# Kernel tuning notes

Measured on AMD Instinct MI355X. Metric: run time of the kernel, lower is better.

## Reference

```python
import jax, jax.numpy as jnp
import numpy as np

T, B, OBS, H, P, L, A = 512, 128, 512, 256, 128, 4, 4


def _ln(x, scale, bias, eps=1e-6):
    mu = jnp.mean(x, axis=-1, keepdims=True)
    var = jnp.mean((x - mu) ** 2, axis=-1, keepdims=True)
    return (x - mu) * jax.lax.rsqrt(var + eps) * scale + bias


def _binop(qi, qj):
    # S5 reset-aware associative operator: elements (A, b, reset_flag)
    Ai, bi, ci = qi
    Aj, bj, cj = qj
    A = (Aj * Ai) * (1.0 - cj) + Aj * cj
    b = (Aj * bi + bj) * (1.0 - cj) + bj * cj
    c = ci * (1.0 - cj) + cj
    return A, b, c


def _s5_layer(x, dones, h0, scale, bias, lam_re, lam_im, b_re, b_im, c_re, c_im, d_vec, log_step, glu_W, glu_b):
    # x: (T,B,H) real, dones: (T,B), h0: (B,P) complex64
    skip = x
    u = _ln(x, scale, bias)                                  # prenorm
    lam = lam_re + 1j * lam_im                               # (P,)
    step = jnp.exp(log_step)                                 # (P,)
    lam_bar = jnp.exp(lam * step)                            # ZOH discretization
    B_bar = ((lam_bar - 1.0) / lam)[:, None] * (b_re + 1j * b_im)  # (P,H)
    Bu = jnp.einsum('tbh,ph->tbp', u.astype(jnp.complex64), B_bar)  # (T,B,P)
    A_el = jnp.concatenate([jnp.ones((1, B, P), jnp.complex64),
                            jnp.broadcast_to(lam_bar.astype(jnp.complex64), (T, B, P))], axis=0)
    b_el = jnp.concatenate([h0[None], Bu], axis=0)
    c_el = jnp.concatenate([jnp.zeros((1, B, 1), jnp.float32), dones[..., None]], axis=0)
    _, xs, _ = jax.lax.associative_scan(_binop, (A_el, b_el, c_el), axis=0)
    xs = xs[1:]                                              # (T,B,P) complex states
    new_h = xs[-1]
    C = c_re + 1j * c_im                                     # (H,P)
    ys = 2.0 * jnp.real(jnp.einsum('tbp,hp->tbh', xs, C)) + d_vec * u  # conj_sym output + D*u
    z = _ln(ys, scale, bias)                                 # gtrxl norm (shared LayerNorm params)
    z = jax.nn.gelu(z)                                       # half_glu1
    z = z * jax.nn.sigmoid(z @ glu_W + glu_b)
    return skip + z, new_h


def setup_inputs() -> dict:
    key = jax.random.key(0)
    ks = jax.random.split(key, 40)
    f32 = jnp.float32

    def n(i, shape, s=1.0):
        return jax.random.normal(ks[i], shape, f32) * s

    inp = {}
    inp['obs'] = n(0, (T, B, OBS))
    inp['dones'] = (jax.random.uniform(ks[1], (T, B)) < 0.01).astype(f32)
    inp['hidden_re'] = jnp.zeros((L, B, P), f32)
    inp['hidden_im'] = jnp.zeros((L, B, P), f32)
    inp['enc0_W'] = n(2, (OBS, 128), 1.0 / np.sqrt(OBS))
    inp['enc0_b'] = jnp.zeros((128,), f32)
    inp['enc1_W'] = n(3, (128, H), 1.0 / np.sqrt(128))
    inp['enc1_b'] = jnp.zeros((H,), f32)
    inp['norm_scale'] = jnp.ones((L, H), f32)
    inp['norm_bias'] = jnp.zeros((L, H), f32)
    inp['Lambda_re'] = -0.5 * jax.random.uniform(ks[4], (L, P), f32) - 0.1
    inp['Lambda_im'] = n(5, (L, P), np.pi)
    inp['B_re'] = n(6, (L, P, H), 1.0 / np.sqrt(H))
    inp['B_im'] = n(7, (L, P, H), 1.0 / np.sqrt(H))
    inp['C_re'] = n(8, (L, H, P), 1.0 / np.sqrt(2 * P))
    inp['C_im'] = n(9, (L, H, P), 1.0 / np.sqrt(2 * P))
    inp['D'] = n(10, (L, H))
    inp['log_step'] = jax.random.uniform(ks[11], (L, P), f32, np.log(1e-3), np.log(1e-1))
    inp['glu_W'] = n(12, (L, H, H), 1.0 / np.sqrt(H))
    inp['glu_b'] = jnp.zeros((L, H), f32)
    inp['ab0_W'] = n(13, (H, 128), 1.0 / np.sqrt(H))
    inp['ab0_b'] = jnp.zeros((128,), f32)
    inp['ab1_W'] = n(14, (128, 128), 1.0 / np.sqrt(128))
    inp['ab1_b'] = jnp.zeros((128,), f32)
    inp['adec_W'] = n(15, (128, A), 0.01 / np.sqrt(128))
    inp['adec_b'] = jnp.full((A,), 0.5, f32)
    inp['log_std'] = jnp.full((A,), -0.7, f32)
    inp['vb0_W'] = n(16, (H, 128), 1.0 / np.sqrt(H))
    inp['vb0_b'] = jnp.zeros((128,), f32)
    inp['vb1_W'] = n(17, (128, 128), 1.0 / np.sqrt(128))
    inp['vb1_b'] = jnp.zeros((128,), f32)
    inp['vdec_W'] = n(18, (128, 1), 1.0 / np.sqrt(128))
    inp['vdec_b'] = jnp.zeros((1,), f32)
    return inp


def reference(obs, dones, hidden_re, hidden_im, enc0_W, enc0_b, enc1_W, enc1_b,
              norm_scale, norm_bias, Lambda_re, Lambda_im, B_re, B_im, C_re, C_im,
              D, log_step, glu_W, glu_b, ab0_W, ab0_b, ab1_W, ab1_b, adec_W, adec_b,
              log_std, vb0_W, vb0_b, vb1_W, vb1_b, vdec_W, vdec_b):
    e = jax.nn.leaky_relu(obs @ enc0_W + enc0_b)
    e = jax.nn.leaky_relu(e @ enc1_W + enc1_b)
    h0 = (hidden_re + 1j * hidden_im).astype(jnp.complex64)  # (L,B,P)
    new_h = []
    for l in range(L):
        e, hl = _s5_layer(e, dones, h0[l], norm_scale[l], norm_bias[l],
                          Lambda_re[l], Lambda_im[l], B_re[l], B_im[l],
                          C_re[l], C_im[l], D[l], log_step[l], glu_W[l], glu_b[l])
        new_h.append(hl)
    new_h = jnp.stack(new_h)
    am = jax.nn.leaky_relu(e @ ab0_W + ab0_b)
    am = jax.nn.leaky_relu(am @ ab1_W + ab1_b)
    am = am @ adec_W + adec_b                                # actor mean (T,B,A)
    v = jax.nn.leaky_relu(e @ vb0_W + vb0_b)
    v = jax.nn.leaky_relu(v @ vb1_W + vb1_b)
    v = v @ vdec_W + vdec_b                                  # critic (T,B,1)
    sc = jnp.broadcast_to(jnp.exp(log_std), am.shape)        # Normal scale (pi params)
    out = jnp.concatenate([am, sc, v], axis=-1)              # (T,B,2A+1)
    return out, jnp.real(new_h), jnp.imag(new_h)
```

## Files before the change

kernel.cpp:

```cpp
#include <hip/hip_runtime.h>
#include <math.h>

#define TT 512
#define BB 128
#define OBSD 512
#define HD 256
#define PD 128
#define LD 4
#define NTB (TT*BB)

typedef __bf16 bf16x8 __attribute__((ext_vector_type(8)));
typedef float  f32x4  __attribute__((ext_vector_type(4)));

__device__ __forceinline__ float bf2f(unsigned short u) {
    return __uint_as_float(((unsigned)u) << 16);
}
__device__ __forceinline__ unsigned short f2bf(float f) {
    unsigned u = __float_as_uint(f);
    unsigned r = (u + 0x7FFFu + ((u >> 16) & 1u)) >> 16;
    return (unsigned short)r;
}
__device__ __forceinline__ float gelu_f(float x) {
    float x3 = x * x * x;
    return 0.5f * x * (1.f + tanhf(0.7978845608028654f * (x + 0.044715f * x3)));
}

template<int MODE, int NJ>
__global__ __launch_bounds__(256, 4) void mgemm2(
    const unsigned short* __restrict__ A, const unsigned short* __restrict__ BT,
    int K, int LDA, const float* __restrict__ bias,
    const float* __restrict__ lnsc, const float* __restrict__ lnbi,
    const unsigned short* __restrict__ aux1, unsigned short* Xio,
    unsigned short* __restrict__ U, int wU)
{
    const int N = NJ * 64;
    __shared__ unsigned short smA[2][64 * 32];
    __shared__ unsigned short smB[2][NJ * 64 * 32];
    float2 (*red)[4] = reinterpret_cast<float2(*)[4]>(&smA[0][0]);
    int tid = threadIdx.x;
    int lane = tid & 63, w = tid >> 6;
    int m16 = lane & 15, quad = lane >> 4;
    int m0 = blockIdx.x * 64;

    f32x4 acc[4][NJ] = {};

    auto stage = [&](int bu, int k0) {
        const unsigned short* g = A + (size_t)(m0 + (tid >> 2)) * LDA + k0 + (tid & 3) * 8;
        __builtin_amdgcn_global_load_lds(
            (const __attribute__((address_space(1))) void*)g,
            (__attribute__((address_space(3))) void*)(&smA[bu][0] + tid * 8), 16, 0, 0);
#pragma unroll
        for (int p = 0; p < NJ; ++p) {
            const unsigned short* gb = BT + (size_t)(p * 64 + (tid >> 2)) * K + k0 + (tid & 3) * 8;
            __builtin_amdgcn_global_load_lds(
                (const __attribute__((address_space(1))) void*)gb,
                (__attribute__((address_space(3))) void*)(&smB[bu][0] + p * 2048 + tid * 8), 16, 0, 0);
        }
    };

    int nk = K >> 5;
    stage(0, 0);
    for (int t = 0; t < nk; ++t) {
        int cur = t & 1;
        if (t + 1 < nk) {
            stage(cur ^ 1, (t + 1) << 5);
            asm volatile("s_waitcnt vmcnt(%0)" :: "i"(NJ + 1) : "memory");
        } else {
            asm volatile("s_waitcnt vmcnt(0)" ::: "memory");
        }
        __builtin_amdgcn_s_barrier();
        __builtin_amdgcn_sched_barrier(0);
        bf16x8 af[4], bfr[NJ];
#pragma unroll
        for (int mi = 0; mi < 4; ++mi)
            af[mi] = *(const bf16x8*)(&smA[cur][0] + (mi * 16 + m16) * 32 + quad * 8);
#pragma unroll
        for (int nj = 0; nj < NJ; ++nj)
            bfr[nj] = *(const bf16x8*)(&smB[cur][0] + (w * NJ * 16 + nj * 16 + m16) * 32 + quad * 8);
#pragma unroll
        for (int mi = 0; mi < 4; ++mi)
#pragma unroll
            for (int nj = 0; nj < NJ; ++nj)
                acc[mi][nj] = __builtin_amdgcn_mfma_f32_16x16x32_bf16(
                    bfr[nj], af[mi], acc[mi][nj], 0, 0, 0);
        __builtin_amdgcn_sched_barrier(0);
        __builtin_amdgcn_s_barrier();
    }

    int colb = w * NJ * 16 + quad * 4;

    if (MODE == 1) {
#pragma unroll
        for (int mi = 0; mi < 4; ++mi) {
            size_t rowb = (size_t)(m0 + mi * 16 + m16) * N;
#pragma unroll
            for (int nj = 0; nj < NJ; ++nj) {
                ushort4 o = { f2bf(acc[mi][nj][0]), f2bf(acc[mi][nj][1]),
                              f2bf(acc[mi][nj][2]), f2bf(acc[mi][nj][3]) };
                *(ushort4*)(U + rowb + colb + nj * 16) = o;
            }
        }
        return;
    }

#pragma unroll
    for (int mi = 0; mi < 4; ++mi) {
        size_t rowb = (size_t)(m0 + mi * 16 + m16) * N;
        float s = 0.f, q = 0.f;
#pragma unroll
        for (int nj = 0; nj < NJ; ++nj) {
            float4 bn = *(const float4*)(bias + colb + nj * 16);
            ushort4 a1, xo;
            if (MODE == 2 || MODE == 3) a1 = *(const ushort4*)(aux1 + rowb + colb + nj * 16);
            if (MODE == 3)              xo = *(const ushort4*)(Xio + rowb + colb + nj * 16);
            float vv[4];
#pragma unroll
            for (int r = 0; r < 4; ++r) {
                float v = acc[mi][nj][r];
                float bv = (r == 0) ? bn.x : (r == 1) ? bn.y : (r == 2) ? bn.z : bn.w;
                if (MODE == 0 || MODE == 4) {
                    v += bv; v = v > 0.f ? v : 0.01f * v;
                } else if (MODE == 2) {
                    float u = bf2f(r == 0 ? a1.x : r == 1 ? a1.y : r == 2 ? a1.z : a1.w);
                    v += bv * u;
                } else if (MODE == 3) {
                    float zz = bf2f(r == 0 ? a1.x : r == 1 ? a1.y : r == 2 ? a1.z : a1.w);
                    float xx = bf2f(r == 0 ? xo.x : r == 1 ? xo.y : r == 2 ? xo.z : xo.w);
                    float sg = 1.f / (1.f + expf(-(v + bv)));
                    v = xx + zz * sg;
                }
                vv[r] = v;
                acc[mi][nj][r] = v;
                s += v; q += v * v;
            }
            if (MODE == 0 || MODE == 3) {
                ushort4 o = { f2bf(vv[0]), f2bf(vv[1]), f2bf(vv[2]), f2bf(vv[3]) };
                *(ushort4*)(Xio + rowb + colb + nj * 16) = o;
            } else if (MODE == 4) {
                ushort4 o = { f2bf(vv[0]), f2bf(vv[1]), f2bf(vv[2]), f2bf(vv[3]) };
                *(ushort4*)(U + rowb + colb + nj * 16) = o;
            }
        }
        if (MODE != 4 && (MODE != 3 || wU)) {
            s += __shfl_xor(s, 16); q += __shfl_xor(q, 16);
            s += __shfl_xor(s, 32); q += __shfl_xor(q, 32);
            if (quad == 0) red[mi * 16 + m16][w] = float2{s, q};
        }
    }
    if (MODE == 4 || (MODE == 3 && !wU)) return;
    __syncthreads();

#pragma unroll
    for (int mi = 0; mi < 4; ++mi) {
        int row_l = mi * 16 + m16;
        float2 t0 = red[row_l][0], t1 = red[row_l][1], t2 = red[row_l][2], t3 = red[row_l][3];
        float S = t0.x + t1.x + t2.x + t3.x;
        float Q = t0.y + t1.y + t2.y + t3.y;
        float mu = S * (1.f / 256.f);
        float var = Q * (1.f / 256.f) - mu * mu;
        float rstd = rsqrtf(var + 1e-6f);
        size_t rowb = (size_t)(m0 + row_l) * N;
#pragma unroll
        for (int nj = 0; nj < NJ; ++nj) {
            float4 ls = *(const float4*)(lnsc + colb + nj * 16);
            float4 lb = *(const float4*)(lnbi + colb + nj * 16);
            float o[4];
#pragma unroll
            for (int r = 0; r < 4; ++r) {
                float sc = (r == 0) ? ls.x : (r == 1) ? ls.y : (r == 2) ? ls.z : ls.w;
                float bi = (r == 0) ? lb.x : (r == 1) ? lb.y : (r == 2) ? lb.z : lb.w;
                float v = (acc[mi][nj][r] - mu) * rstd * sc + bi;
                if (MODE == 2) v = gelu_f(v);
                o[r] = v;
            }
            ushort4 ov = { f2bf(o[0]), f2bf(o[1]), f2bf(o[2]), f2bf(o[3]) };
            *(ushort4*)(U + rowb + colb + nj * 16) = ov;
        }
    }
}

__global__ __launch_bounds__(256, 4) void mgemm_obs(
    const float* __restrict__ A, const unsigned short* __restrict__ BT,
    unsigned short* __restrict__ U, const float* __restrict__ bias)
{
    const int K = 512, NJ = 2, N = 128;
    __shared__ unsigned short smA[64 * 32];
    __shared__ unsigned short smB[NJ * 64 * 32];
    int tid = threadIdx.x;
    int lane = tid & 63, w = tid >> 6;
    int m16 = lane & 15, quad = lane >> 4;
    int m0 = blockIdx.x * 64;

    f32x4 acc[4][NJ] = {};
    for (int k0 = 0; k0 < K; k0 += 32) {
#pragma unroll
        for (int p = 0; p < 2; ++p) {
            int idx = p * 256 + tid;
            int r = idx >> 3, kq = (idx & 7) * 4;
            float4 v = *(const float4*)(A + (size_t)(m0 + r) * K + k0 + kq);
            ushort4 o = { f2bf(v.x), f2bf(v.y), f2bf(v.z), f2bf(v.w) };
            *(ushort4*)(smA + r * 32 + kq) = o;
        }
#pragma unroll
        for (int p = 0; p < NJ; ++p) {
            const unsigned short* g = BT + (size_t)(p * 64 + (tid >> 2)) * K + k0 + (tid & 3) * 8;
            unsigned short* l = smB + p * 2048 + tid * 8;
            __builtin_amdgcn_global_load_lds(
                (const __attribute__((address_space(1))) void*)g,
                (__attribute__((address_space(3))) void*)l, 16, 0, 0);
        }
        __syncthreads();
        bf16x8 af[4], bfr[NJ];
#pragma unroll
        for (int mi = 0; mi < 4; ++mi)
            af[mi] = *(const bf16x8*)(smA + (mi * 16 + m16) * 32 + quad * 8);
#pragma unroll
        for (int nj = 0; nj < NJ; ++nj)
            bfr[nj] = *(const bf16x8*)(smB + (w * NJ * 16 + nj * 16 + m16) * 32 + quad * 8);
#pragma unroll
        for (int mi = 0; mi < 4; ++mi)
#pragma unroll
            for (int nj = 0; nj < NJ; ++nj)
                acc[mi][nj] = __builtin_amdgcn_mfma_f32_16x16x32_bf16(
                    bfr[nj], af[mi], acc[mi][nj], 0, 0, 0);
        __syncthreads();
    }
    int colb = w * NJ * 16 + quad * 4;
#pragma unroll
    for (int mi = 0; mi < 4; ++mi) {
        size_t rowb = (size_t)(m0 + mi * 16 + m16) * N;
#pragma unroll
        for (int nj = 0; nj < NJ; ++nj) {
            float4 bv = *(const float4*)(bias + colb + nj * 16);
            float v0 = acc[mi][nj][0] + bv.x; v0 = v0 > 0.f ? v0 : 0.01f * v0;
            float v1 = acc[mi][nj][1] + bv.y; v1 = v1 > 0.f ? v1 : 0.01f * v1;
            float v2 = acc[mi][nj][2] + bv.z; v2 = v2 > 0.f ? v2 : 0.01f * v2;
            float v3 = acc[mi][nj][3] + bv.w; v3 = v3 > 0.f ? v3 : 0.01f * v3;
            ushort4 o = { f2bf(v0), f2bf(v1), f2bf(v2), f2bf(v3) };
            *(ushort4*)(U + rowb + colb + nj * 16) = o;
        }
    }
}

__global__ __launch_bounds__(512) void scan2_k(
    const unsigned short* __restrict__ bu, unsigned short* __restrict__ xs,
    const float* __restrict__ dones,
    const float* __restrict__ h0re, const float* __restrict__ h0im,
    const float* __restrict__ lamre, const float* __restrict__ lamim,
    const float* __restrict__ lstep,
    float* __restrict__ outre, float* __restrict__ outim)
{
    __shared__ float sdone[TT];
    __shared__ float4 ssum[8][64];
    __shared__ float2 shin[8][64];
    int tid = threadIdx.x;
    int b  = blockIdx.x >> 1;
    int ph = blockIdx.x & 1;
    int chunk = tid >> 6, pl = tid & 63;
    int p = ph * 64 + pl;
    sdone[tid] = dones[tid * BB + b];
    float lr = lamre[p], li = lamim[p];
    float st = expf(lstep[p]);
    float er = expf(lr * st);
    float ar = er * cosf(li * st);
    float ai = er * sinf(li * st);
    __syncthreads();

    int t0 = chunk * 64;
    unsigned buf[64];
    float Ar = 1.f, Ai = 0.f, br = 0.f, bi = 0.f;
#pragma unroll
    for (int j = 0; j < 64; ++j) {
        size_t off = ((size_t)(t0 + j) * BB + b) * 256 + 2 * p;
        unsigned v = *(const unsigned*)(bu + off);
        buf[j] = v;
        float bur = bf2f((unsigned short)(v & 0xFFFFu));
        float bui = bf2f((unsigned short)(v >> 16));
        if (sdone[t0 + j] != 0.f) {
            Ar = 0.f; Ai = 0.f; br = bur; bi = bui;
        } else {
            float nAr = ar * Ar - ai * Ai;
            float nAi = ar * Ai + ai * Ar;
            float nbr = fmaf(ar, br, fmaf(-ai, bi, bur));
            float nbi = fmaf(ar, bi, fmaf(ai, br, bui));
            Ar = nAr; Ai = nAi; br = nbr; bi = nbi;
        }
    }
    ssum[chunk][pl] = float4{Ar, Ai, br, bi};
    __syncthreads();
    if (tid < 64) {
        int gid = b * 128 + p;
        float hr = h0re[gid], hi = h0im[gid];
#pragma unroll
        for (int c = 0; c < 8; ++c) {
            shin[c][pl] = float2{hr, hi};
            float4 s = ssum[c][pl];
            float nhr = fmaf(s.x, hr, fmaf(-s.y, hi, s.z));
            float nhi = fmaf(s.x, hi, fmaf(s.y, hr, s.w));
            hr = nhr; hi = nhi;
        }
        outre[gid] = hr; outim[gid] = hi;
    }
    __syncthreads();
    float hr = shin[chunk][pl].x, hi = shin[chunk][pl].y;
#pragma unroll
    for (int j = 0; j < 64; ++j) {
        unsigned v = buf[j];
        float bur = bf2f((unsigned short)(v & 0xFFFFu));
        float bui = bf2f((unsigned short)(v >> 16));
        float nr, ni;
        if (sdone[t0 + j] != 0.f) { nr = bur; ni = bui; }
        else {
            nr = fmaf(ar, hr, fmaf(-ai, hi, bur));
            ni = fmaf(ar, hi, fmaf(ai, hr, bui));
        }
        hr = nr; hi = ni;
        size_t off = ((size_t)(t0 + j) * BB + b) * 256 + 2 * p;
        *(unsigned*)(xs + off) = ((unsigned)f2bf(ni) << 16) | f2bf(nr);
    }
}

__global__ __launch_bounds__(256) void prep_k(
    const float* __restrict__ Br, const float* __restrict__ Bi,
    const float* __restrict__ Cr, const float* __restrict__ Ci,
    const float* __restrict__ Lr, const float* __restrict__ Li,
    const float* __restrict__ ls, unsigned short* bbarT, unsigned short* ccatT)
{
    int gid = blockIdx.x * 256 + threadIdx.x;
    int l = gid >> 15;
    int rem = gid & 32767;
    int p = rem >> 8;
    int h = rem & 255;
    float lr = Lr[l * PD + p], li = Li[l * PD + p];
    float st = expf(ls[l * PD + p]);
    float er = expf(lr * st);
    float lbr = er * cosf(li * st);
    float lbi = er * sinf(li * st);
    float nr = lbr - 1.f, ni = lbi;
    float den = lr * lr + li * li;
    float fr = (nr * lr + ni * li) / den;
    float fi = (ni * lr - nr * li) / den;
    float bre = Br[(size_t)(l * PD + p) * HD + h];
    float bim = Bi[(size_t)(l * PD + p) * HD + h];
    size_t lb = (size_t)l * 65536;
    bbarT[lb + (size_t)(2 * p) * 256 + h]     = f2bf(fr * bre - fi * bim);
    bbarT[lb + (size_t)(2 * p + 1) * 256 + h] = f2bf(fr * bim + fi * bre);
    float cre = Cr[(size_t)(l * HD + h) * PD + p];
    float cim = Ci[(size_t)(l * HD + h) * PD + p];
    ccatT[lb + (size_t)h * 256 + 2 * p]     = f2bf(2.f * cre);
    ccatT[lb + (size_t)h * 256 + 2 * p + 1] = f2bf(-2.f * cim);
}

__global__ __launch_bounds__(256) void tcvt_k(const float* __restrict__ in,
    unsigned short* __restrict__ out, int K, int N)
{
    int gid = blockIdx.x * 256 + threadIdx.x;
    if (gid >= K * N) return;
    int k = gid / N, n = gid - k * N;
    out[(size_t)n * K + k] = f2bf(in[gid]);
}

__global__ __launch_bounds__(256) void tcvt4_k(const float* __restrict__ in,
    unsigned short* __restrict__ out)
{
    int gid = blockIdx.x * 256 + threadIdx.x;
    int l = gid >> 16;
    int rem = gid & 65535;
    int k = rem >> 8, n = rem & 255;
    out[(size_t)l * 65536 + (size_t)n * 256 + k] = f2bf(in[gid]);
}

__global__ __launch_bounds__(256) void catb_k(const float* __restrict__ a,
    const float* __restrict__ b, float* __restrict__ out)
{
    int i = threadIdx.x;
    out[i] = (i < 128) ? a[i] : b[i - 128];
}

__global__ __launch_bounds__(256) void head_k(
    const unsigned short* __restrict__ am2, const unsigned short* __restrict__ v2,
    const float* __restrict__ adW, const float* __restrict__ adb,
    const float* __restrict__ lstd,
    const float* __restrict__ vdW, const float* __restrict__ vdb,
    float* out)
{
    int wid = threadIdx.x >> 6, lane = threadIdx.x & 63;
    size_t row = (size_t)blockIdx.x * 4 + wid;
    float a1 = bf2f(am2[row * 128 + lane]);
    float a2 = bf2f(am2[row * 128 + 64 + lane]);
    float w1 = bf2f(v2[row * 128 + lane]);
    float w2 = bf2f(v2[row * 128 + 64 + lane]);
    float vals[5];
#pragma unroll
    for (int a = 0; a < 4; ++a)
        vals[a] = a1 * adW[lane * 4 + a] + a2 * adW[(lane + 64) * 4 + a];
    vals[4] = w1 * vdW[lane] + w2 * vdW[64 + lane];
#pragma unroll
    for (int off = 32; off; off >>= 1)
#pragma unroll
        for (int k = 0; k < 5; ++k) vals[k] += __shfl_xor(vals[k], off);
    if (lane == 0) {
        size_t o = row * 9;
#pragma unroll
        for (int a = 0; a < 4; ++a) out[o + a] = vals[a] + adb[a];
#pragma unroll
        for (int a = 0; a < 4; ++a) out[o + 4 + a] = expf(lstd[a]);
        out[o + 8] = vals[4] + vdb[0];
    }
}

extern "C" void kernel_launch(void* const* d_in, const int* in_sizes, int n_in,
                              void* d_out, int out_size, void* d_ws, size_t ws_size,
                              hipStream_t stream) {
    (void)in_sizes; (void)n_in; (void)out_size; (void)ws_size;
    const float* obs     = (const float*)d_in[0];
    const float* dones   = (const float*)d_in[1];
    const float* hre     = (const float*)d_in[2];
    const float* him     = (const float*)d_in[3];
    const float* enc0_W  = (const float*)d_in[4];
    const float* enc0_b  = (const float*)d_in[5];
    const float* enc1_W  = (const float*)d_in[6];
    const float* enc1_b  = (const float*)d_in[7];
    const float* nsc     = (const float*)d_in[8];
    const float* nbi     = (const float*)d_in[9];
    const float* Lre     = (const float*)d_in[10];
    const float* Lim     = (const float*)d_in[11];
    const float* B_re    = (const float*)d_in[12];
    const float* B_im    = (const float*)d_in[13];
    const float* C_re    = (const float*)d_in[14];
    const float* C_im    = (const float*)d_in[15];
    const float* Dv      = (const float*)d_in[16];
    const float* lstep   = (const float*)d_in[17];
    const float* glu_W   = (const float*)d_in[18];
    const float* glu_b   = (const float*)d_in[19];
    const float* ab0_W   = (const float*)d_in[20];
    const float* ab0_b   = (const float*)d_in[21];
    const float* ab1_W   = (const float*)d_in[22];
    const float* ab1_b   = (const float*)d_in[23];
    const float* adec_W  = (const float*)d_in[24];
    const float* adec_b  = (const float*)d_in[25];
    const float* log_std = (const float*)d_in[26];
    const float* vb0_W   = (const float*)d_in[27];
    const float* vb0_b   = (const float*)d_in[28];
    const float* vb1_W   = (const float*)d_in[29];
    const float* vb1_b   = (const float*)d_in[30];
    const float* vdec_W  = (const float*)d_in[31];
    const float* vdec_b  = (const float*)d_in[32];

    const size_t MB = (size_t)1 << 20;
    char* wsb = (char*)d_ws;
    unsigned short* XS    = (unsigned short*)(wsb);
    unsigned short* AMV1  = (unsigned short*)(wsb);
    unsigned short* AM2   = (unsigned short*)(wsb + 32 * MB);
    unsigned short* V2    = (unsigned short*)(wsb + 48 * MB);
    unsigned short* U1    = (unsigned short*)(wsb + 64 * MB);
    unsigned short* X     = (unsigned short*)(wsb + 96 * MB);
    unsigned short* U     = (unsigned short*)(wsb + 128 * MB);
    unsigned short* BU    = (unsigned short*)(wsb + 160 * MB);
    char* wgt = wsb + 192 * MB;
    unsigned short* BBART = (unsigned short*)(wgt);
    unsigned short* CCATT = (unsigned short*)(wgt + 512 * 1024);
    unsigned short* GLUT  = (unsigned short*)(wgt + 1024 * 1024);
    unsigned short* E0T   = (unsigned short*)(wgt + 1536 * 1024);
    unsigned short* E1T   = (unsigned short*)(wgt + 1664 * 1024);
    unsigned short* AB0VT = (unsigned short*)(wgt + 1728 * 1024);
    unsigned short* AB1T  = (unsigned short*)(wgt + 1856 * 1024);
    unsigned short* VB1T  = (unsigned short*)(wgt + 1888 * 1024);
    float*          CB0   = (float*)(wgt + 1920 * 1024);

    float* out   = (float*)d_out;
    float* outre = out + (size_t)NTB * 9;
    float* outim = outre + LD * BB * PD;

    prep_k<<<512, 256, 0, stream>>>(B_re, B_im, C_re, C_im, Lre, Lim, lstep, BBART, CCATT);
    tcvt_k<<<256, 256, 0, stream>>>(enc0_W, E0T, 512, 128);
    tcvt_k<<<128, 256, 0, stream>>>(enc1_W, E1T, 128, 256);
    tcvt4_k<<<1024, 256, 0, stream>>>(glu_W, GLUT);
    tcvt_k<<<128, 256, 0, stream>>>(ab0_W, AB0VT, 256, 128);
    tcvt_k<<<128, 256, 0, stream>>>(vb0_W, AB0VT + 128 * 256, 256, 128);
    tcvt_k<<<64, 256, 0, stream>>>(ab1_W, AB1T, 128, 128);
    tcvt_k<<<64, 256, 0, stream>>>(vb1_W, VB1T, 128, 128);
    catb_k<<<1, 256, 0, stream>>>(ab0_b, vb0_b, CB0);

    mgemm_obs<<<1024, 256, 0, stream>>>(obs, E0T, U1, enc0_b);
    mgemm2<0, 4><<<1024, 256, 0, stream>>>(U1, E1T, 128, 128, enc1_b, nsc, nbi, nullptr, X, U, 1);

    for (int l = 0; l < LD; ++l) {
        mgemm2<1, 4><<<1024, 256, 0, stream>>>(U, BBART + (size_t)l * 65536, 256, 256,
                                               nullptr, nullptr, nullptr, nullptr, nullptr, BU, 0);
        scan2_k<<<256, 512, 0, stream>>>(BU, XS, dones, hre + l * BB * PD, him + l * BB * PD,
                                         Lre + l * PD, Lim + l * PD, lstep + l * PD,
                                         outre + l * BB * PD, outim + l * BB * PD);
        mgemm2<2, 4><<<1024, 256, 0, stream>>>(XS, CCATT + (size_t)l * 65536, 256, 256,
                                               Dv + l * HD, nsc + l * HD, nbi + l * HD, U, nullptr, U, 1);
        const float* nsc2 = nsc + ((l + 1 < LD) ? (l + 1) * HD : 0);
        const float* nbi2 = nbi + ((l + 1 < LD) ? (l + 1) * HD : 0);
        mgemm2<3, 4><<<1024, 256, 0, stream>>>(U, GLUT + (size_t)l * 65536, 256, 256,
                                               glu_b + l * HD, nsc2, nbi2, U, X, U, (l + 1 < LD) ? 1 : 0);
    }

    mgemm2<4, 4><<<1024, 256, 0, stream>>>(X, AB0VT, 256, 256, CB0, nullptr, nullptr, nullptr, nullptr, AMV1, 0);
    mgemm2<4, 2><<<1024, 256, 0, stream>>>(AMV1, AB1T, 128, 256, ab1_b, nullptr, nullptr, nullptr, nullptr, AM2, 0);
    mgemm2<4, 2><<<1024, 256, 0, stream>>>(AMV1 + 128, VB1T, 128, 256, vb1_b, nullptr, nullptr, nullptr, nullptr, V2, 0);
    head_k<<<NTB / 4, 256, 0, stream>>>(AM2, V2, adec_W, adec_b, log_std, vdec_W, vdec_b, out);
}
```

Before: 1.048 ms.

## Use 8-wave GEMM blocks with triple-buffered LDS prefetch

Result: faster. 960.5 us (-8.4%).

```diff
diff --git a/kernel.cpp b/kernel.cpp
--- a/kernel.cpp
+++ b/kernel.cpp
@@ -26,75 +26,95 @@
 }
 
 template<int MODE, int NJ>
-__global__ __launch_bounds__(256, 4) void mgemm2(
+__global__ __launch_bounds__(512) void mgemm2(
     const unsigned short* __restrict__ A, const unsigned short* __restrict__ BT,
     int K, int LDA, const float* __restrict__ bias,
     const float* __restrict__ lnsc, const float* __restrict__ lnbi,
     const unsigned short* __restrict__ aux1, unsigned short* Xio,
     unsigned short* __restrict__ U, int wU)
 {
+    constexpr int NJW = NJ / 2;
+    constexpr int LPS = 2 + NJW;
     const int N = NJ * 64;
-    __shared__ unsigned short smA[2][64 * 32];
-    __shared__ unsigned short smB[2][NJ * 64 * 32];
-    float2 (*red)[4] = reinterpret_cast<float2(*)[4]>(&smA[0][0]);
+    __shared__ unsigned short smA[3 * 2048];
+    __shared__ unsigned short smB[3 * NJ * 2048];
+    float2 (*red)[8] = reinterpret_cast<float2(*)[8]>(&smA[0]);
     int tid = threadIdx.x;
     int lane = tid & 63, w = tid >> 6;
     int m16 = lane & 15, quad = lane >> 4;
     int m0 = blockIdx.x * 64;
 
-    f32x4 acc[4][NJ] = {};
-
-    auto stage = [&](int bu, int k0) {
-        const unsigned short* g = A + (size_t)(m0 + (tid >> 2)) * LDA + k0 + (tid & 3) * 8;
-        __builtin_amdgcn_global_load_lds(
-            (const __attribute__((address_space(1))) void*)g,
-            (__attribute__((address_space(3))) void*)(&smA[bu][0] + tid * 8), 16, 0, 0);
-#pragma unroll
-        for (int p = 0; p < NJ; ++p) {
-            const unsigned short* gb = BT + (size_t)(p * 64 + (tid >> 2)) * K + k0 + (tid & 3) * 8;
+    f32x4 acc[4][NJW] = {};
+
+    auto stage = [&](int slot, int kt) {
+        int k0 = kt << 5;
+#pragma unroll
+        for (int j = 0; j < 2; ++j) {
+            int chunk = w * 2 + j;
+            int e = chunk * 128 + lane * 2;
+            int row = e >> 5, kb = e & 31;
+            const unsigned short* g = A + (size_t)(m0 + row) * LDA + k0 + kb;
             __builtin_amdgcn_global_load_lds(
-                (const __attribute__((address_space(1))) void*)gb,
-                (__attribute__((address_space(3))) void*)(&smB[bu][0] + p * 2048 + tid * 8), 16, 0, 0);
+                (const __attribute__((address_space(1))) void*)g,
+                (__attribute__((address_space(3))) void*)(smA + slot * 2048 + chunk * 128 + lane * 2),
+                4, 0, 0);
+        }
+#pragma unroll
+        for (int j = 0; j < NJW; ++j) {
+            int chunk = w * NJW + j;
+            int e = chunk * 512 + lane * 8;
+            int p = e >> 11, r = (e >> 5) & 63, kq = e & 31;
+            const unsigned short* g = BT + (size_t)(p * 64 + r) * K + k0 + kq;
+            __builtin_amdgcn_global_load_lds(
+                (const __attribute__((address_space(1))) void*)g,
+                (__attribute__((address_space(3))) void*)(smB + slot * NJ * 2048 + chunk * 512 + lane * 8),
+                16, 0, 0);
         }
     };
 
     int nk = K >> 5;
     stage(0, 0);
+    stage(1, 1);
+    int cur = 0, nxt = 2;
     for (int t = 0; t < nk; ++t) {
-        int cur = t & 1;
-        if (t + 1 < nk) {
-            stage(cur ^ 1, (t + 1) << 5);
-            asm volatile("s_waitcnt vmcnt(%0)" :: "i"(NJ + 1) : "memory");
+        int rem = nk - 1 - t;
+        if (rem >= 2) {
+            stage(nxt, t + 2);
+            nxt = (nxt == 2) ? 0 : nxt + 1;
+            asm volatile("s_waitcnt vmcnt(%0)" :: "i"(2 * LPS) : "memory");
+        } else if (rem == 1) {
+            asm volatile("s_waitcnt vmcnt(%0)" :: "i"(LPS) : "memory");
         } else {
             asm volatile("s_waitcnt vmcnt(0)" ::: "memory");
         }
         __builtin_amdgcn_s_barrier();
         __builtin_amdgcn_sched_barrier(0);
-        bf16x8 af[4], bfr[NJ];
+        bf16x8 af[4], bfr[NJW];
 #pragma unroll
         for (int mi = 0; mi < 4; ++mi)
-            af[mi] = *(const bf16x8*)(&smA[cur][0] + (mi * 16 + m16) * 32 + quad * 8);
-#pragma unroll
-        for (int nj = 0; nj < NJ; ++nj)
-            bfr[nj] = *(const bf16x8*)(&smB[cur][0] + (w * NJ * 16 + nj * 16 + m16) * 32 + quad * 8);
+            af[mi] = *(const bf16x8*)(smA + cur * 2048 + (mi * 16 + m16) * 32 + quad * 8);
+#pragma unroll
+        for (int nj = 0; nj < NJW; ++nj)
+            bfr[nj] = *(const bf16x8*)(smB + cur * NJ * 2048 + (w * NJW + nj) * 512 + m16 * 32 + quad * 8);
 #pragma unroll
         for (int mi = 0; mi < 4; ++mi)
 #pragma unroll
-            for (int nj = 0; nj < NJ; ++nj)
+            for (int nj = 0; nj < NJW; ++nj)
                 acc[mi][nj] = __builtin_amdgcn_mfma_f32_16x16x32_bf16(
                     bfr[nj], af[mi], acc[mi][nj], 0, 0, 0);
         __builtin_amdgcn_sched_barrier(0);
         __builtin_amdgcn_s_barrier();
-    }
-
-    int colb = w * NJ * 16 + quad * 4;
+        cur = (cur == 2) ? 0 : cur + 1;
+    }
+
+    int colb = w * (NJW * 16) + quad * 4;
 
     if (MODE == 1) {
 #pragma unroll
         for (int mi = 0; mi < 4; ++mi) {
             size_t rowb = (size_t)(m0 + mi * 16 + m16) * N;
 #pragma unroll
-            for (int nj = 0; nj < NJ; ++nj) {
+            for (int nj = 0; nj < NJW; ++nj) {
                 ushort4 o = { f2bf(acc[mi][nj][0]), f2bf(acc[mi][nj][1]),
                               f2bf(acc[mi][nj][2]), f2bf(acc[mi][nj][3]) };
                 *(ushort4*)(U + rowb + colb + nj * 16) = o;
@@ -108,7 +128,7 @@
         size_t rowb = (size_t)(m0 + mi * 16 + m16) * N;
         float s = 0.f, q = 0.f;
 #pragma unroll
-        for (int nj = 0; nj < NJ; ++nj) {
+        for (int nj = 0; nj < NJW; ++nj) {
             float4 bn = *(const float4*)(bias + colb + nj * 16);
             ushort4 a1, xo;
             if (MODE == 2 || MODE == 3) a1 = *(const ushort4*)(aux1 + rowb + colb + nj * 16);
@@ -153,15 +173,18 @@
 #pragma unroll
     for (int mi = 0; mi < 4; ++mi) {
         int row_l = mi * 16 + m16;
-        float2 t0 = red[row_l][0], t1 = red[row_l][1], t2 = red[row_l][2], t3 = red[row_l][3];
-        float S = t0.x + t1.x + t2.x + t3.x;
-        float Q = t0.y + t1.y + t2.y + t3.y;
+        float S = 0.f, Q = 0.f;
+#pragma unroll
+        for (int ww = 0; ww < 8; ++ww) {
+            float2 tv = red[row_l][ww];
+            S += tv.x; Q += tv.y;
+        }
         float mu = S * (1.f / 256.f);
         float var = Q * (1.f / 256.f) - mu * mu;
         float rstd = rsqrtf(var + 1e-6f);
         size_t rowb = (size_t)(m0 + row_l) * N;
 #pragma unroll
-        for (int nj = 0; nj < NJ; ++nj) {
+        for (int nj = 0; nj < NJW; ++nj) {
             float4 ls = *(const float4*)(lnsc + colb + nj * 16);
             float4 lb = *(const float4*)(lnbi + colb + nj * 16);
             float o[4];
@@ -179,7 +202,7 @@
     }
 }
 
-__global__ __launch_bounds__(256, 4) void mgemm_obs(
+__global__ __launch_bounds__(256) void mgemm_obs(
     const float* __restrict__ A, const unsigned short* __restrict__ BT,
     unsigned short* __restrict__ U, const float* __restrict__ bias)
 {
@@ -483,24 +506,24 @@
     catb_k<<<1, 256, 0, stream>>>(ab0_b, vb0_b, CB0);
 
     mgemm_obs<<<1024, 256, 0, stream>>>(obs, E0T, U1, enc0_b);
-    mgemm2<0, 4><<<1024, 256, 0, stream>>>(U1, E1T, 128, 128, enc1_b, nsc, nbi, nullptr, X, U, 1);
+    mgemm2<0, 4><<<1024, 512, 0, stream>>>(U1, E1T, 128, 128, enc1_b, nsc, nbi, nullptr, X, U, 1);
 
     for (int l = 0; l < LD; ++l) {
-        mgemm2<1, 4><<<1024, 256, 0, stream>>>(U, BBART + (size_t)l * 65536, 256, 256,
+        mgemm2<1, 4><<<1024, 512, 0, stream>>>(U, BBART + (size_t)l * 65536, 256, 256,
                                                nullptr, nullptr, nullptr, nullptr, nullptr, BU, 0);
         scan2_k<<<256, 512, 0, stream>>>(BU, XS, dones, hre + l * BB * PD, him + l * BB * PD,
                                          Lre + l * PD, Lim + l * PD, lstep + l * PD,
                                          outre + l * BB * PD, outim + l * BB * PD);
-        mgemm2<2, 4><<<1024, 256, 0, stream>>>(XS, CCATT + (size_t)l * 65536, 256, 256,
+        mgemm2<2, 4><<<1024, 512, 0, stream>>>(XS, CCATT + (size_t)l * 65536, 256, 256,
                                                Dv + l * HD, nsc + l * HD, nbi + l * HD, U, nullptr, U, 1);
         const float* nsc2 = nsc + ((l + 1 < LD) ? (l + 1) * HD : 0);
         const float* nbi2 = nbi + ((l + 1 < LD) ? (l + 1) * HD : 0);
-        mgemm2<3, 4><<<1024, 256, 0, stream>>>(U, GLUT + (size_t)l * 65536, 256, 256,
+        mgemm2<3, 4><<<1024, 512, 0, stream>>>(U, GLUT + (size_t)l * 65536, 256, 256,
                                                glu_b + l * HD, nsc2, nbi2, U, X, U, (l + 1 < LD) ? 1 : 0);
     }
 
-    mgemm2<4, 4><<<1024, 256, 0, stream>>>(X, AB0VT, 256, 256, CB0, nullptr, nullptr, nullptr, nullptr, AMV1, 0);
-    mgemm2<4, 2><<<1024, 256, 0, stream>>>(AMV1, AB1T, 128, 256, ab1_b, nullptr, nullptr, nullptr, nullptr, AM2, 0);
-    mgemm2<4, 2><<<1024, 256, 0, stream>>>(AMV1 + 128, VB1T, 128, 256, vb1_b, nullptr, nullptr, nullptr, nullptr, V2, 0);
+    mgemm2<4, 4><<<1024, 512, 0, stream>>>(X, AB0VT, 256, 256, CB0, nullptr, nullptr, nullptr, nullptr, AMV1, 0);
+    mgemm2<4, 2><<<1024, 512, 0, stream>>>(AMV1, AB1T, 128, 256, ab1_b, nullptr, nullptr, nullptr, nullptr, AM2, 0);
+    mgemm2<4, 2><<<1024, 512, 0, stream>>>(AMV1 + 128, VB1T, 128, 256, vb1_b, nullptr, nullptr, nullptr, nullptr, V2, 0);
     head_k<<<NTB / 4, 256, 0, stream>>>(AM2, V2, adec_W, adec_b, log_std, vdec_W, vdec_b, out);
 }
```
